# Kernel tuning notes

Measured on AMD Instinct MI355X. Metric: run time of the kernel, lower is better.

The kernel has to match this reference:

```python
import jax, jax.numpy as jnp
import numpy as np

N = 16          # num_transforms
BS = 128        # batch_size
D = 4096        # encoder dim
C, H, W = 3, 64, 64
TEMP = 0.5      # hyperparams.temperature
LAM_H = 1.0     # hyperparams.h
EPS = 1e-8      # torch CosineSimilarity eps


def setup_inputs() -> dict:
    key = jax.random.key(0)
    k1, k2, k3 = jax.random.split(key, 3)
    return {
        "pic_set": jax.random.normal(k1, (N, BS, C, H, W), dtype=jnp.float32),
        "dec_pics": jax.random.normal(k2, (N, BS, C, H, W), dtype=jnp.float32),
        "h": jax.random.normal(k3, (N, BS, D), dtype=jnp.float32),
    }


def _pos_neg_indices(n, bs):
    # Static (numpy) index construction replicating the boolean masks.
    # Positives of row i: all j != i with j % bs == i % bs (sorted, row-major),
    # Negatives of row i: all j with j % bs != i % bs (sorted).
    k = n * bs
    i = np.arange(k)
    cols = (i % bs)[:, None] + np.arange(n)[None, :] * bs          # (K, N)
    pos_idx = cols[cols != i[:, None]].reshape(k, n - 1)            # (K, N-1)
    jj = np.arange(k)
    neg_mask = (jj[None, :] % bs) != (i[:, None] % bs)              # (K, K)
    neg_idx = np.broadcast_to(jj, (k, k))[neg_mask].reshape(k, k - n)  # (K, K-N)
    return jnp.asarray(pos_idx), jnp.asarray(neg_idx)


def _nt_xent(h):
    n, bs, d = h.shape
    k = n * bs
    s = h.reshape(k, d)
    # CosineSimilarity(dim=2) with eps clamp on norms
    nrm = jnp.maximum(jnp.linalg.norm(s, axis=1), EPS)
    sn = s / nrm[:, None]
    simmat = (sn @ sn.T) / TEMP                                     # (K, K)
    pos_idx, neg_idx = _pos_neg_indices(n, bs)
    pos = jnp.take_along_axis(simmat, pos_idx, axis=1)              # (K, N-1)
    neg = jnp.take_along_axis(simmat, neg_idx, axis=1)              # (K, K-N)
    # CrossEntropyLoss(reduction='sum') with label 0 on logits
    # [pos_{i,m}, neg_i] == sum of logsumexp - pos; logsumexp over concat
    # factors as logaddexp(lse(neg_i), pos_{i,m}).
    neg_lse = jax.scipy.special.logsumexp(neg, axis=1)              # (K,)
    loss = jnp.sum(jnp.logaddexp(neg_lse[:, None], pos) - pos)
    kpos = k * (n - 1)
    return loss / kpos


def reference(pic_set, dec_pics, h):
    n, bs = pic_set.shape[0], pic_set.shape[1]
    loss_h = _nt_xent(h)
    # dec_pics[(i+1) % N] cyclic offset, then flat MSE (mean reduction)
    offset = (np.arange(n) + 1) % n
    p = pic_set.reshape(n, bs, -1)
    dshift = dec_pics.reshape(n, bs, -1)[offset]
    loss_pairs = jnp.mean((p - dshift) ** 2)
    return loss_pairs + LAM_H * loss_h
```

## Files before the change

### kernel.cpp

```cpp
#include <hip/hip_runtime.h>
#include <hip/hip_bf16.h>
#include <math.h>

#define N_T   16
#define BSZ   128
#define DDIM  4096
#define KROWS (N_T * BSZ)
#define CHW   (3 * 64 * 64)
#define S_PIC (BSZ * CHW)
#define T_MSE (N_T * S_PIC)
#define KPOS  (KROWS * (N_T - 1))

#define MSE_BLOCKS  3072

typedef short  bf16x8 __attribute__((ext_vector_type(8)));
typedef float  f32x4  __attribute__((ext_vector_type(4)));

__device__ __forceinline__ float waveReduceSum(float v) {
    for (int off = 32; off > 0; off >>= 1) v += __shfl_down(v, off, 64);
    return v;
}
__device__ __forceinline__ float blockReduceSum(float v) {
    __shared__ float s[8];
    int lane = threadIdx.x & 63, wid = threadIdx.x >> 6;
    v = waveReduceSum(v);
    if (lane == 0) s[wid] = v;
    __syncthreads();
    int nw = (blockDim.x + 63) >> 6;
    v = (threadIdx.x < nw) ? s[threadIdx.x] : 0.0f;
    if (wid == 0) v = waveReduceSum(v);
    return v;
}

__device__ __forceinline__ void mse_block(const float* __restrict__ pic,
                                          const float* __restrict__ dec,
                                          float* __restrict__ acc,
                                          int n, int bx) {
    const size_t off = (size_t)n * S_PIC + (size_t)bx * 8192 + threadIdx.x * 4;
    const ptrdiff_t doff = (ptrdiff_t)(((n + 1) & (N_T - 1)) - n) * S_PIC;
    const float* p = pic + off;
    const float* d = dec + off + doff;
    float s0 = 0.f, s1 = 0.f, s2 = 0.f, s3 = 0.f;
#pragma unroll
    for (int k = 0; k < 8; k++) {
        float4 a = *(const float4*)(p + k * 1024);
        float4 b = *(const float4*)(d + k * 1024);
        float dx = a.x - b.x, dy = a.y - b.y, dz = a.z - b.z, dw = a.w - b.w;
        s0 += dx * dx; s1 += dy * dy; s2 += dz * dz; s3 += dw * dw;
    }
    float sum = (s0 + s1) + (s2 + s3);
    sum = blockReduceSum(sum);
    if (threadIdx.x == 0) atomicAdd(acc, sum);
}

__global__ void norm_kernel(const float* __restrict__ h,
                            __hip_bfloat16* __restrict__ hb,
                            float* __restrict__ acc, int zero_acc) {
    if (zero_acc && blockIdx.x == 0 && threadIdx.x < 64)
        acc[threadIdx.x] = 0.0f;

    const int row = blockIdx.x;
    const float* r = h + (size_t)row * DDIM;
    float ss = 0.0f;
    for (int k = threadIdx.x * 8; k < DDIM; k += blockDim.x * 8) {
        float4 v0 = *(const float4*)(r + k);
        float4 v1 = *(const float4*)(r + k + 4);
        ss += v0.x * v0.x + v0.y * v0.y + v0.z * v0.z + v0.w * v0.w;
        ss += v1.x * v1.x + v1.y * v1.y + v1.z * v1.z + v1.w * v1.w;
    }
    ss = blockReduceSum(ss);
    __shared__ float scale_s;
    if (threadIdx.x == 0) scale_s = 1.0f / fmaxf(sqrtf(ss), 1e-8f);
    __syncthreads();
    const float sc = scale_s;
    __hip_bfloat16* ob = hb + (size_t)row * DDIM;
    for (int k = threadIdx.x * 8; k < DDIM; k += blockDim.x * 8) {
        float4 v0 = *(const float4*)(r + k);
        float4 v1 = *(const float4*)(r + k + 4);
        __hip_bfloat16 t[8];
        t[0] = __float2bfloat16(v0.x * sc); t[1] = __float2bfloat16(v0.y * sc);
        t[2] = __float2bfloat16(v0.z * sc); t[3] = __float2bfloat16(v0.w * sc);
        t[4] = __float2bfloat16(v1.x * sc); t[5] = __float2bfloat16(v1.y * sc);
        t[6] = __float2bfloat16(v1.z * sc); t[7] = __float2bfloat16(v1.w * sc);
        *(bf16x8*)(ob + k) = *(const bf16x8*)t;
    }
}

template<int NKZ>
__global__ __launch_bounds__(256) void mega_kernel(const ushort* __restrict__ X,
                                                   float* __restrict__ Cpart,
                                                   const float* __restrict__ pic,
                                                   const float* __restrict__ dec,
                                                   float* __restrict__ acc) {
    __shared__ ushort As[128 * 32];
    __shared__ ushort Bs[128 * 32];
    constexpr int NG = NKZ * 256;
    int bid = blockIdx.x;

    if (bid >= NG) {
        const int t = bid - NG;
        mse_block(pic, dec, acc, t & (N_T - 1), t >> 4);
        return;
    }

    bid = (bid & 7) * (NG >> 3) + (bid >> 3);

    const int kz = bid >> 8;
    const int bi = (bid >> 4) & 15, bj = bid & 15;
    const int tid  = threadIdx.x;
    const int wave = tid >> 6, lane = tid & 63;
    const int wm = wave >> 1, wn = wave & 1;
    const int quad = lane >> 4, l16 = lane & 15;

    f32x4 acc_r[4][4];
#pragma unroll
    for (int i = 0; i < 4; i++)
#pragma unroll
        for (int j = 0; j < 4; j++) acc_r[i][j] = (f32x4){0.f, 0.f, 0.f, 0.f};

    const int srow = lane >> 2;
    const int scol = (lane & 3) * 8;
    const ushort* Ag0 = X + (size_t)(bi * 128 + wave * 16       + srow) * DDIM + scol;
    const ushort* Ag1 = X + (size_t)(bi * 128 + (wave + 4) * 16 + srow) * DDIM + scol;
    const ushort* Bg0 = X + (size_t)(bj * 128 + wave * 16       + srow) * DDIM + scol;
    const ushort* Bg1 = X + (size_t)(bj * 128 + (wave + 4) * 16 + srow) * DDIM + scol;
    ushort* Al0 = As + wave * 512;
    ushort* Al1 = As + (wave + 4) * 512;
    ushort* Bl0 = Bs + wave * 512;
    ushort* Bl1 = Bs + (wave + 4) * 512;

    constexpr int KS = DDIM / NKZ;
    const int k0 = kz * KS, k1 = k0 + KS;
    for (int kk = k0; kk < k1; kk += 32) {
        __syncthreads();
        __builtin_amdgcn_global_load_lds(
            (const __attribute__((address_space(1))) unsigned int*)(Ag0 + kk),
            (__attribute__((address_space(3))) unsigned int*)Al0, 16, 0, 0);
        __builtin_amdgcn_global_load_lds(
            (const __attribute__((address_space(1))) unsigned int*)(Ag1 + kk),
            (__attribute__((address_space(3))) unsigned int*)Al1, 16, 0, 0);
        __builtin_amdgcn_global_load_lds(
            (const __attribute__((address_space(1))) unsigned int*)(Bg0 + kk),
            (__attribute__((address_space(3))) unsigned int*)Bl0, 16, 0, 0);
        __builtin_amdgcn_global_load_lds(
            (const __attribute__((address_space(1))) unsigned int*)(Bg1 + kk),
            (__attribute__((address_space(3))) unsigned int*)Bl1, 16, 0, 0);
        __syncthreads();

        bf16x8 a[4], b[4];
#pragma unroll
        for (int t = 0; t < 4; t++)
            a[t] = *(const bf16x8*)(As + (wm * 64 + t * 16 + l16) * 32 + quad * 8);
#pragma unroll
        for (int t = 0; t < 4; t++)
            b[t] = *(const bf16x8*)(Bs + (wn * 64 + t * 16 + l16) * 32 + quad * 8);
#pragma unroll
        for (int mt = 0; mt < 4; mt++)
#pragma unroll
            for (int nt = 0; nt < 4; nt++)
                acc_r[mt][nt] = __builtin_amdgcn_mfma_f32_16x16x32_bf16(
                    a[mt], b[nt], acc_r[mt][nt], 0, 0, 0);
    }

    float* Cp = Cpart + (size_t)kz * KROWS * KROWS;
#pragma unroll
    for (int mt = 0; mt < 4; mt++) {
#pragma unroll
        for (int r = 0; r < 4; r++) {
            const int row = bi * 128 + wm * 64 + mt * 16 + quad * 4 + r;
            float* o = Cp + (size_t)row * KROWS + bj * 128 + wn * 64 + l16;
#pragma unroll
            for (int nt = 0; nt < 4; nt++) o[nt * 16] = 2.0f * acc_r[mt][nt][r];
        }
    }
}

__global__ __launch_bounds__(256) void mse_kernel(const float* __restrict__ pic,
                                                  const float* __restrict__ dec,
                                                  float* __restrict__ acc) {
    mse_block(pic, dec, acc, blockIdx.y, blockIdx.x);
}

template<int NKZ>
__global__ void lse_kernel(const float* __restrict__ Cpart,
                           float* __restrict__ acc,
                           float* __restrict__ out) {
    const int i = blockIdx.x;
    __shared__ float srow[KROWS];
    const float* r0 = Cpart + (size_t)i * KROWS;
    for (int j = threadIdx.x * 4; j < KROWS; j += blockDim.x * 4) {
        float4 s = *(const float4*)(r0 + j);
#pragma unroll
        for (int p = 1; p < NKZ; p++) {
            float4 b = *(const float4*)(r0 + (size_t)p * KROWS * KROWS + j);
            s.x += b.x; s.y += b.y; s.z += b.z; s.w += b.w;
        }
        *(float4*)(srow + j) = s;
    }
    __syncthreads();

    const int ires = i & (BSZ - 1);
    float se = 0.0f;
    for (int j = threadIdx.x; j < KROWS; j += blockDim.x)
        if ((j & (BSZ - 1)) != ires) se += __expf(srow[j] - 2.0f);
    se = blockReduceSum(se);

    if (threadIdx.x == 0) {
        const float neg_lse = 2.0f + __logf(se);
        float loss = 0.0f;
#pragma unroll
        for (int t = 0; t < N_T; t++) {
            const int j = ires + t * BSZ;
            if (j == i) continue;
            const float x = neg_lse - srow[j];
            loss += (x > 0.0f) ? (x + log1pf(expf(-x))) : log1pf(expf(x));
        }
        atomicAdd(acc + 1, loss);
        __threadfence();
        const int old = atomicAdd((int*)acc + 8, 1);
        if (old == KROWS - 1) {
            const float mse = atomicAdd(acc + 0, 0.0f);
            const float lh  = atomicAdd(acc + 1, 0.0f);
            out[0] = mse / (float)T_MSE + lh / (float)KPOS;
        }
    }
}

extern "C" void kernel_launch(void* const* d_in, const int* in_sizes, int n_in,
                              void* d_out, int out_size, void* d_ws, size_t ws_size,
                              hipStream_t stream) {
    const float* pic = (const float*)d_in[0];
    float* dec = (float*)d_in[1];
    const float* h = (const float*)d_in[2];
    float* out = (float*)d_out;

    float* acc = (float*)d_ws;
    const size_t hbuf_bytes = (size_t)KROWS * DDIM * sizeof(__hip_bfloat16);
    const size_t part_bytes = (size_t)KROWS * KROWS * sizeof(float);

    if (ws_size >= 256 + hbuf_bytes + 4 * part_bytes) {
        __hip_bfloat16* hbuf = (__hip_bfloat16*)((char*)d_ws + 256);
        float* Cpart = (float*)((char*)d_ws + 256 + hbuf_bytes);
        norm_kernel<<<KROWS, 256, 0, stream>>>(h, hbuf, acc, 1);
        mega_kernel<4><<<4 * 256 + MSE_BLOCKS, 256, 0, stream>>>(
            (const ushort*)hbuf, Cpart, pic, dec, acc);
        lse_kernel<4><<<KROWS, 256, 0, stream>>>(Cpart, acc, out);
    } else if (ws_size >= 256 + hbuf_bytes + 2 * part_bytes) {
        __hip_bfloat16* hbuf = (__hip_bfloat16*)((char*)d_ws + 256);
        float* Cpart = (float*)((char*)d_ws + 256 + hbuf_bytes);
        norm_kernel<<<KROWS, 256, 0, stream>>>(h, hbuf, acc, 1);
        mega_kernel<2><<<2 * 256 + MSE_BLOCKS, 256, 0, stream>>>(
            (const ushort*)hbuf, Cpart, pic, dec, acc);
        lse_kernel<2><<<KROWS, 256, 0, stream>>>(Cpart, acc, out);
    } else {
        hipMemsetAsync(d_ws, 0, 256, stream);
        __hip_bfloat16* hbuf = (__hip_bfloat16*)dec;
        float* Cpart = (float*)((char*)dec + hbuf_bytes);
        mse_kernel<<<dim3(MSE_BLOCKS / N_T, N_T), 256, 0, stream>>>(pic, dec, acc);
        norm_kernel<<<KROWS, 256, 0, stream>>>(h, hbuf, acc, 0);
        mega_kernel<2><<<2 * 256, 256, 0, stream>>>(
            (const ushort*)hbuf, Cpart, pic, dec, acc);
        lse_kernel<2><<<KROWS, 256, 0, stream>>>(Cpart, acc, out);
    }
}
```

Before: 345.2 us.

## Fuse norm, GEMM, MSE and LSE into one persistent kernel with grid barriers

```diff
diff --git a/kernel.cpp b/kernel.cpp
--- a/kernel.cpp
+++ b/kernel.cpp
@@ -11,6 +11,8 @@
 #define T_MSE (N_T * S_PIC)
 #define KPOS  (KROWS * (N_T - 1))
 
+#define NBLK        1024
+#define MSE_JOBS    3072
 #define MSE_BLOCKS  3072
 
 typedef short  bf16x8 __attribute__((ext_vector_type(8)));
@@ -22,25 +24,44 @@
 }
 __device__ __forceinline__ float blockReduceSum(float v) {
     __shared__ float s[8];
+    __syncthreads();
     int lane = threadIdx.x & 63, wid = threadIdx.x >> 6;
     v = waveReduceSum(v);
     if (lane == 0) s[wid] = v;
     __syncthreads();
-    int nw = (blockDim.x + 63) >> 6;
-    v = (threadIdx.x < nw) ? s[threadIdx.x] : 0.0f;
+    v = (threadIdx.x < 4) ? s[threadIdx.x] : 0.0f;
     if (wid == 0) v = waveReduceSum(v);
     return v;
 }
 
-__device__ __forceinline__ void mse_block(const float* __restrict__ pic,
-                                          const float* __restrict__ dec,
-                                          float* __restrict__ acc,
-                                          int n, int bx) {
+__device__ __forceinline__ void grid_sync(int* cnt, int* gen) {
+    __syncthreads();
+    __threadfence();
+    __syncthreads();
+    if (threadIdx.x == 0) {
+        const int g = __hip_atomic_load(gen, __ATOMIC_RELAXED, __HIP_MEMORY_SCOPE_AGENT);
+        if (__hip_atomic_fetch_add(cnt, 1, __ATOMIC_ACQ_REL, __HIP_MEMORY_SCOPE_AGENT)
+            == NBLK - 1) {
+            __hip_atomic_store(cnt, 0, __ATOMIC_RELAXED, __HIP_MEMORY_SCOPE_AGENT);
+            __hip_atomic_fetch_add(gen, 1, __ATOMIC_RELEASE, __HIP_MEMORY_SCOPE_AGENT);
+        } else {
+            while (__hip_atomic_load(gen, __ATOMIC_ACQUIRE, __HIP_MEMORY_SCOPE_AGENT) == g)
+                __builtin_amdgcn_s_sleep(8);
+        }
+    }
+    __syncthreads();
+    __threadfence();
+}
+
+__device__ __forceinline__ void mse_job(const float* __restrict__ pic,
+                                        const float* __restrict__ dec,
+                                        int t, float& s0, float& s1,
+                                        float& s2, float& s3) {
+    const int n = t & (N_T - 1), bx = t >> 4;
     const size_t off = (size_t)n * S_PIC + (size_t)bx * 8192 + threadIdx.x * 4;
     const ptrdiff_t doff = (ptrdiff_t)(((n + 1) & (N_T - 1)) - n) * S_PIC;
     const float* p = pic + off;
     const float* d = dec + off + doff;
-    float s0 = 0.f, s1 = 0.f, s2 = 0.f, s3 = 0.f;
 #pragma unroll
     for (int k = 0; k < 8; k++) {
         float4 a = *(const float4*)(p + k * 1024);
@@ -48,8 +69,189 @@
         float dx = a.x - b.x, dy = a.y - b.y, dz = a.z - b.z, dw = a.w - b.w;
         s0 += dx * dx; s1 += dy * dy; s2 += dz * dz; s3 += dw * dw;
     }
-    float sum = (s0 + s1) + (s2 + s3);
-    sum = blockReduceSum(sum);
+}
+
+__global__ __launch_bounds__(256, 4) void fused_kernel(
+        const float* __restrict__ pic, const float* __restrict__ dec,
+        const float* __restrict__ h, __hip_bfloat16* __restrict__ hbuf,
+        float* __restrict__ Cpart, float* __restrict__ acc,
+        int* __restrict__ bar, float* __restrict__ out) {
+    __shared__ ushort As[128 * 32];
+    __shared__ ushort Bs[128 * 32];
+    __shared__ float scale_s;
+    const int tid = threadIdx.x;
+    int* const cnt = bar;
+    int* const gen = bar + 1;
+
+    {
+        const ushort* hu = (const ushort*)h;
+        (void)hu;
+#pragma unroll
+        for (int rr = 0; rr < 2; rr++) {
+            const int row = (blockIdx.x << 1) | rr;
+            const float* rp = h + (size_t)row * DDIM + tid * 16;
+            float4 v0 = *(const float4*)(rp);
+            float4 v1 = *(const float4*)(rp + 4);
+            float4 v2 = *(const float4*)(rp + 8);
+            float4 v3 = *(const float4*)(rp + 12);
+            float ss = v0.x * v0.x + v0.y * v0.y + v0.z * v0.z + v0.w * v0.w
+                     + v1.x * v1.x + v1.y * v1.y + v1.z * v1.z + v1.w * v1.w
+                     + v2.x * v2.x + v2.y * v2.y + v2.z * v2.z + v2.w * v2.w
+                     + v3.x * v3.x + v3.y * v3.y + v3.z * v3.z + v3.w * v3.w;
+            ss = blockReduceSum(ss);
+            if (tid == 0) scale_s = 1.0f / fmaxf(sqrtf(ss), 1e-8f);
+            __syncthreads();
+            const float sc = scale_s;
+            __hip_bfloat16 t[16];
+            t[0]  = __float2bfloat16(v0.x * sc); t[1]  = __float2bfloat16(v0.y * sc);
+            t[2]  = __float2bfloat16(v0.z * sc); t[3]  = __float2bfloat16(v0.w * sc);
+            t[4]  = __float2bfloat16(v1.x * sc); t[5]  = __float2bfloat16(v1.y * sc);
+            t[6]  = __float2bfloat16(v1.z * sc); t[7]  = __float2bfloat16(v1.w * sc);
+            t[8]  = __float2bfloat16(v2.x * sc); t[9]  = __float2bfloat16(v2.y * sc);
+            t[10] = __float2bfloat16(v2.z * sc); t[11] = __float2bfloat16(v2.w * sc);
+            t[12] = __float2bfloat16(v3.x * sc); t[13] = __float2bfloat16(v3.y * sc);
+            t[14] = __float2bfloat16(v3.z * sc); t[15] = __float2bfloat16(v3.w * sc);
+            __hip_bfloat16* ob = hbuf + (size_t)row * DDIM + tid * 16;
+            *(bf16x8*)(ob)     = *(const bf16x8*)(t);
+            *(bf16x8*)(ob + 8) = *(const bf16x8*)(t + 8);
+        }
+        float s0 = 0.f, s1 = 0.f, s2 = 0.f, s3 = 0.f;
+#pragma unroll
+        for (int q = 0; q < 3; q++)
+            mse_job(pic, dec, blockIdx.x * 3 + q, s0, s1, s2, s3);
+        float msum = blockReduceSum((s0 + s1) + (s2 + s3));
+        if (tid == 0) atomicAdd(acc, msum);
+    }
+
+    grid_sync(cnt, gen);
+
+    {
+        int bid = blockIdx.x;
+        bid = (bid & 7) * (NBLK >> 3) + (bid >> 3);
+        const int kz = bid >> 8;
+        const int bi = (bid >> 4) & 15, bj = bid & 15;
+        const int wave = tid >> 6, lane = tid & 63;
+        const int wm = wave >> 1, wn = wave & 1;
+        const int quad = lane >> 4, l16 = lane & 15;
+        const ushort* X = (const ushort*)hbuf;
+
+        f32x4 acc_r[4][4];
+#pragma unroll
+        for (int i = 0; i < 4; i++)
+#pragma unroll
+            for (int j = 0; j < 4; j++) acc_r[i][j] = (f32x4){0.f, 0.f, 0.f, 0.f};
+
+        const int srw = lane >> 2;
+        const int scl = (lane & 3) * 8;
+        const ushort* Ag0 = X + (size_t)(bi * 128 + wave * 16       + srw) * DDIM + scl;
+        const ushort* Ag1 = X + (size_t)(bi * 128 + (wave + 4) * 16 + srw) * DDIM + scl;
+        const ushort* Bg0 = X + (size_t)(bj * 128 + wave * 16       + srw) * DDIM + scl;
+        const ushort* Bg1 = X + (size_t)(bj * 128 + (wave + 4) * 16 + srw) * DDIM + scl;
+        ushort* Al0 = As + wave * 512;
+        ushort* Al1 = As + (wave + 4) * 512;
+        ushort* Bl0 = Bs + wave * 512;
+        ushort* Bl1 = Bs + (wave + 4) * 512;
+
+        const int k0 = kz * (DDIM / 4), k1 = k0 + (DDIM / 4);
+        for (int kk = k0; kk < k1; kk += 32) {
+            __syncthreads();
+            __builtin_amdgcn_global_load_lds(
+                (const __attribute__((address_space(1))) unsigned int*)(Ag0 + kk),
+                (__attribute__((address_space(3))) unsigned int*)Al0, 16, 0, 0);
+            __builtin_amdgcn_global_load_lds(
+                (const __attribute__((address_space(1))) unsigned int*)(Ag1 + kk),
+                (__attribute__((address_space(3))) unsigned int*)Al1, 16, 0, 0);
+            __builtin_amdgcn_global_load_lds(
+                (const __attribute__((address_space(1))) unsigned int*)(Bg0 + kk),
+                (__attribute__((address_space(3))) unsigned int*)Bl0, 16, 0, 0);
+            __builtin_amdgcn_global_load_lds(
+                (const __attribute__((address_space(1))) unsigned int*)(Bg1 + kk),
+                (__attribute__((address_space(3))) unsigned int*)Bl1, 16, 0, 0);
+            __syncthreads();
+
+            bf16x8 a[4], b[4];
+#pragma unroll
+            for (int t = 0; t < 4; t++)
+                a[t] = *(const bf16x8*)(As + (wm * 64 + t * 16 + l16) * 32 + quad * 8);
+#pragma unroll
+            for (int t = 0; t < 4; t++)
+                b[t] = *(const bf16x8*)(Bs + (wn * 64 + t * 16 + l16) * 32 + quad * 8);
+#pragma unroll
+            for (int mt = 0; mt < 4; mt++)
+#pragma unroll
+                for (int nt = 0; nt < 4; nt++)
+                    acc_r[mt][nt] = __builtin_amdgcn_mfma_f32_16x16x32_bf16(
+                        a[mt], b[nt], acc_r[mt][nt], 0, 0, 0);
+        }
+
+        float* Cp = Cpart + (size_t)kz * KROWS * KROWS;
+#pragma unroll
+        for (int mt = 0; mt < 4; mt++) {
+#pragma unroll
+            for (int r = 0; r < 4; r++) {
+                const int row = bi * 128 + wm * 64 + mt * 16 + quad * 4 + r;
+                float* o = Cp + (size_t)row * KROWS + bj * 128 + wn * 64 + l16;
+#pragma unroll
+                for (int nt = 0; nt < 4; nt++) o[nt * 16] = 2.0f * acc_r[mt][nt][r];
+            }
+        }
+    }
+
+    grid_sync(cnt, gen);
+
+    {
+        float* srow = (float*)As;
+        float lsum = 0.0f;
+#pragma unroll
+        for (int rr = 0; rr < 2; rr++) {
+            const int i = (blockIdx.x << 1) | rr;
+            __syncthreads();
+            const float* r0 = Cpart + (size_t)i * KROWS;
+            for (int j = tid * 4; j < KROWS; j += 1024) {
+                float4 s = *(const float4*)(r0 + j);
+#pragma unroll
+                for (int p = 1; p < 4; p++) {
+                    const float4 b = *(const float4*)(r0 + (size_t)p * KROWS * KROWS + j);
+                    s.x += b.x; s.y += b.y; s.z += b.z; s.w += b.w;
+                }
+                *(float4*)(srow + j) = s;
+            }
+            __syncthreads();
+            const int ires = i & (BSZ - 1);
+            float se = 0.0f;
+            for (int j = tid; j < KROWS; j += 256)
+                if ((j & (BSZ - 1)) != ires) se += __expf(srow[j] - 2.0f);
+            se = blockReduceSum(se);
+            if (tid == 0) {
+                const float neg_lse = 2.0f + __logf(se);
+#pragma unroll
+                for (int t = 0; t < N_T; t++) {
+                    const int j = ires + t * BSZ;
+                    if (j == i) continue;
+                    const float x = neg_lse - srow[j];
+                    lsum += (x > 0.0f) ? (x + log1pf(expf(-x))) : log1pf(expf(x));
+                }
+            }
+        }
+        if (tid == 0) atomicAdd(acc + 1, lsum);
+    }
+
+    grid_sync(cnt, gen);
+
+    if (blockIdx.x == 0 && threadIdx.x == 0) {
+        const float mse = atomicAdd(acc + 0, 0.0f);
+        const float lh  = atomicAdd(acc + 1, 0.0f);
+        out[0] = mse / (float)T_MSE + lh / (float)KPOS;
+    }
+}
+
+__device__ __forceinline__ void mse_block(const float* __restrict__ pic,
+                                          const float* __restrict__ dec,
+                                          float* __restrict__ acc,
+                                          int n, int bx) {
+    float s0 = 0.f, s1 = 0.f, s2 = 0.f, s3 = 0.f;
+    mse_job(pic, dec, (bx << 4) | n, s0, s1, s2, s3);
+    float sum = blockReduceSum((s0 + s1) + (s2 + s3));
     if (threadIdx.x == 0) atomicAdd(acc, sum);
 }
 
@@ -58,7 +260,6 @@
                             float* __restrict__ acc, int zero_acc) {
     if (zero_acc && blockIdx.x == 0 && threadIdx.x < 64)
         acc[threadIdx.x] = 0.0f;
-
     const int row = blockIdx.x;
     const float* r = h + (size_t)row * DDIM;
     float ss = 0.0f;
@@ -96,39 +297,33 @@
     __shared__ ushort Bs[128 * 32];
     constexpr int NG = NKZ * 256;
     int bid = blockIdx.x;
-
     if (bid >= NG) {
         const int t = bid - NG;
         mse_block(pic, dec, acc, t & (N_T - 1), t >> 4);
         return;
     }
-
     bid = (bid & 7) * (NG >> 3) + (bid >> 3);
-
     const int kz = bid >> 8;
     const int bi = (bid >> 4) & 15, bj = bid & 15;
-    const int tid  = threadIdx.x;
+    const int tid = threadIdx.x;
     const int wave = tid >> 6, lane = tid & 63;
     const int wm = wave >> 1, wn = wave & 1;
     const int quad = lane >> 4, l16 = lane & 15;
-
     f32x4 acc_r[4][4];
 #pragma unroll
     for (int i = 0; i < 4; i++)
 #pragma unroll
         for (int j = 0; j < 4; j++) acc_r[i][j] = (f32x4){0.f, 0.f, 0.f, 0.f};
-
-    const int srow = lane >> 2;
-    const int scol = (lane & 3) * 8;
-    const ushort* Ag0 = X + (size_t)(bi * 128 + wave * 16       + srow) * DDIM + scol;
-    const ushort* Ag1 = X + (size_t)(bi * 128 + (wave + 4) * 16 + srow) * DDIM + scol;
-    const ushort* Bg0 = X + (size_t)(bj * 128 + wave * 16       + srow) * DDIM + scol;
-    const ushort* Bg1 = X + (size_t)(bj * 128 + (wave + 4) * 16 + srow) * DDIM + scol;
+    const int srw = lane >> 2;
+    const int scl = (lane & 3) * 8;
+    const ushort* Ag0 = X + (size_t)(bi * 128 + wave * 16       + srw) * DDIM + scl;
+    const ushort* Ag1 = X + (size_t)(bi * 128 + (wave + 4) * 16 + srw) * DDIM + scl;
+    const ushort* Bg0 = X + (size_t)(bj * 128 + wave * 16       + srw) * DDIM + scl;
+    const ushort* Bg1 = X + (size_t)(bj * 128 + (wave + 4) * 16 + srw) * DDIM + scl;
     ushort* Al0 = As + wave * 512;
     ushort* Al1 = As + (wave + 4) * 512;
     ushort* Bl0 = Bs + wave * 512;
     ushort* Bl1 = Bs + (wave + 4) * 512;
-
     constexpr int KS = DDIM / NKZ;
     const int k0 = kz * KS, k1 = k0 + KS;
     for (int kk = k0; kk < k1; kk += 32) {
@@ -146,7 +341,6 @@
             (const __attribute__((address_space(1))) unsigned int*)(Bg1 + kk),
             (__attribute__((address_space(3))) unsigned int*)Bl1, 16, 0, 0);
         __syncthreads();
-
         bf16x8 a[4], b[4];
 #pragma unroll
         for (int t = 0; t < 4; t++)
@@ -161,7 +355,6 @@
                 acc_r[mt][nt] = __builtin_amdgcn_mfma_f32_16x16x32_bf16(
                     a[mt], b[nt], acc_r[mt][nt], 0, 0, 0);
     }
-
     float* Cp = Cpart + (size_t)kz * KROWS * KROWS;
 #pragma unroll
     for (int mt = 0; mt < 4; mt++) {
@@ -198,13 +391,11 @@
         *(float4*)(srow + j) = s;
     }
     __syncthreads();
-
     const int ires = i & (BSZ - 1);
     float se = 0.0f;
     for (int j = threadIdx.x; j < KROWS; j += blockDim.x)
         if ((j & (BSZ - 1)) != ires) se += __expf(srow[j] - 2.0f);
     se = blockReduceSum(se);
-
     if (threadIdx.x == 0) {
         const float neg_lse = 2.0f + __logf(se);
         float loss = 0.0f;
@@ -235,16 +426,15 @@
     float* out = (float*)d_out;
 
     float* acc = (float*)d_ws;
+    int* bar = (int*)d_ws + 32;
     const size_t hbuf_bytes = (size_t)KROWS * DDIM * sizeof(__hip_bfloat16);
     const size_t part_bytes = (size_t)KROWS * KROWS * sizeof(float);
 
     if (ws_size >= 256 + hbuf_bytes + 4 * part_bytes) {
         __hip_bfloat16* hbuf = (__hip_bfloat16*)((char*)d_ws + 256);
         float* Cpart = (float*)((char*)d_ws + 256 + hbuf_bytes);
-        norm_kernel<<<KROWS, 256, 0, stream>>>(h, hbuf, acc, 1);
-        mega_kernel<4><<<4 * 256 + MSE_BLOCKS, 256, 0, stream>>>(
-            (const ushort*)hbuf, Cpart, pic, dec, acc);
-        lse_kernel<4><<<KROWS, 256, 0, stream>>>(Cpart, acc, out);
+        hipMemsetAsync(d_ws, 0, 256, stream);
+        fused_kernel<<<NBLK, 256, 0, stream>>>(pic, dec, h, hbuf, Cpart, acc, bar, out);
     } else if (ws_size >= 256 + hbuf_bytes + 2 * part_bytes) {
         __hip_bfloat16* hbuf = (__hip_bfloat16*)((char*)d_ws + 256);
         float* Cpart = (float*)((char*)d_ws + 256 + hbuf_bytes);
```

Result: slower. 1.359 ms (+293.6%).

## Double-buffer GEMM LDS tiles, drop 4-way split-K path, flatten norm kernel

Applied to the files above, without the earlier changes.

```diff
diff --git a/kernel.cpp b/kernel.cpp
--- a/kernel.cpp
+++ b/kernel.cpp
@@ -53,37 +53,40 @@
     if (threadIdx.x == 0) atomicAdd(acc, sum);
 }
 
-__global__ void norm_kernel(const float* __restrict__ h,
-                            __hip_bfloat16* __restrict__ hb,
-                            float* __restrict__ acc, int zero_acc) {
+__global__ __launch_bounds__(256) void norm_kernel(const float* __restrict__ h,
+                                                   __hip_bfloat16* __restrict__ hb,
+                                                   float* __restrict__ acc,
+                                                   int zero_acc) {
     if (zero_acc && blockIdx.x == 0 && threadIdx.x < 64)
         acc[threadIdx.x] = 0.0f;
 
     const int row = blockIdx.x;
-    const float* r = h + (size_t)row * DDIM;
-    float ss = 0.0f;
-    for (int k = threadIdx.x * 8; k < DDIM; k += blockDim.x * 8) {
-        float4 v0 = *(const float4*)(r + k);
-        float4 v1 = *(const float4*)(r + k + 4);
-        ss += v0.x * v0.x + v0.y * v0.y + v0.z * v0.z + v0.w * v0.w;
-        ss += v1.x * v1.x + v1.y * v1.y + v1.z * v1.z + v1.w * v1.w;
-    }
+    const float* rp = h + (size_t)row * DDIM + threadIdx.x * 16;
+    float4 v0 = *(const float4*)(rp);
+    float4 v1 = *(const float4*)(rp + 4);
+    float4 v2 = *(const float4*)(rp + 8);
+    float4 v3 = *(const float4*)(rp + 12);
+    float ss = v0.x * v0.x + v0.y * v0.y + v0.z * v0.z + v0.w * v0.w
+             + v1.x * v1.x + v1.y * v1.y + v1.z * v1.z + v1.w * v1.w
+             + v2.x * v2.x + v2.y * v2.y + v2.z * v2.z + v2.w * v2.w
+             + v3.x * v3.x + v3.y * v3.y + v3.z * v3.z + v3.w * v3.w;
     ss = blockReduceSum(ss);
     __shared__ float scale_s;
     if (threadIdx.x == 0) scale_s = 1.0f / fmaxf(sqrtf(ss), 1e-8f);
     __syncthreads();
     const float sc = scale_s;
-    __hip_bfloat16* ob = hb + (size_t)row * DDIM;
-    for (int k = threadIdx.x * 8; k < DDIM; k += blockDim.x * 8) {
-        float4 v0 = *(const float4*)(r + k);
-        float4 v1 = *(const float4*)(r + k + 4);
-        __hip_bfloat16 t[8];
-        t[0] = __float2bfloat16(v0.x * sc); t[1] = __float2bfloat16(v0.y * sc);
-        t[2] = __float2bfloat16(v0.z * sc); t[3] = __float2bfloat16(v0.w * sc);
-        t[4] = __float2bfloat16(v1.x * sc); t[5] = __float2bfloat16(v1.y * sc);
-        t[6] = __float2bfloat16(v1.z * sc); t[7] = __float2bfloat16(v1.w * sc);
-        *(bf16x8*)(ob + k) = *(const bf16x8*)t;
-    }
+    __hip_bfloat16 t[16];
+    t[0]  = __float2bfloat16(v0.x * sc); t[1]  = __float2bfloat16(v0.y * sc);
+    t[2]  = __float2bfloat16(v0.z * sc); t[3]  = __float2bfloat16(v0.w * sc);
+    t[4]  = __float2bfloat16(v1.x * sc); t[5]  = __float2bfloat16(v1.y * sc);
+    t[6]  = __float2bfloat16(v1.z * sc); t[7]  = __float2bfloat16(v1.w * sc);
+    t[8]  = __float2bfloat16(v2.x * sc); t[9]  = __float2bfloat16(v2.y * sc);
+    t[10] = __float2bfloat16(v2.z * sc); t[11] = __float2bfloat16(v2.w * sc);
+    t[12] = __float2bfloat16(v3.x * sc); t[13] = __float2bfloat16(v3.y * sc);
+    t[14] = __float2bfloat16(v3.z * sc); t[15] = __float2bfloat16(v3.w * sc);
+    __hip_bfloat16* ob = hb + (size_t)row * DDIM + threadIdx.x * 16;
+    *(bf16x8*)(ob)     = *(const bf16x8*)(t);
+    *(bf16x8*)(ob + 8) = *(const bf16x8*)(t + 8);
 }
 
 template<int NKZ>
@@ -92,8 +95,10 @@
                                                    const float* __restrict__ pic,
                                                    const float* __restrict__ dec,
                                                    float* __restrict__ acc) {
-    __shared__ ushort As[128 * 32];
-    __shared__ ushort Bs[128 * 32];
+    __shared__ ushort As0[128 * 32];
+    __shared__ ushort Bs0[128 * 32];
+    __shared__ ushort As1[128 * 32];
+    __shared__ ushort Bs1[128 * 32];
     constexpr int NG = NKZ * 256;
     int bid = blockIdx.x;
 
@@ -118,48 +123,63 @@
 #pragma unroll
         for (int j = 0; j < 4; j++) acc_r[i][j] = (f32x4){0.f, 0.f, 0.f, 0.f};
 
-    const int srow = lane >> 2;
-    const int scol = (lane & 3) * 8;
-    const ushort* Ag0 = X + (size_t)(bi * 128 + wave * 16       + srow) * DDIM + scol;
-    const ushort* Ag1 = X + (size_t)(bi * 128 + (wave + 4) * 16 + srow) * DDIM + scol;
-    const ushort* Bg0 = X + (size_t)(bj * 128 + wave * 16       + srow) * DDIM + scol;
-    const ushort* Bg1 = X + (size_t)(bj * 128 + (wave + 4) * 16 + srow) * DDIM + scol;
-    ushort* Al0 = As + wave * 512;
-    ushort* Al1 = As + (wave + 4) * 512;
-    ushort* Bl0 = Bs + wave * 512;
-    ushort* Bl1 = Bs + (wave + 4) * 512;
-
-    constexpr int KS = DDIM / NKZ;
-    const int k0 = kz * KS, k1 = k0 + KS;
-    for (int kk = k0; kk < k1; kk += 32) {
-        __syncthreads();
+    const int srw = lane >> 2;
+    const int scl = (lane & 3) * 8;
+    const ushort* Ag0 = X + (size_t)(bi * 128 + wave * 16       + srw) * DDIM + scl;
+    const ushort* Ag1 = X + (size_t)(bi * 128 + (wave + 4) * 16 + srw) * DDIM + scl;
+    const ushort* Bg0 = X + (size_t)(bj * 128 + wave * 16       + srw) * DDIM + scl;
+    const ushort* Bg1 = X + (size_t)(bj * 128 + (wave + 4) * 16 + srw) * DDIM + scl;
+
+    auto stage = [&](ushort* Al, ushort* Bl, int kk) {
         __builtin_amdgcn_global_load_lds(
             (const __attribute__((address_space(1))) unsigned int*)(Ag0 + kk),
-            (__attribute__((address_space(3))) unsigned int*)Al0, 16, 0, 0);
+            (__attribute__((address_space(3))) unsigned int*)(Al + wave * 512), 16, 0, 0);
         __builtin_amdgcn_global_load_lds(
             (const __attribute__((address_space(1))) unsigned int*)(Ag1 + kk),
-            (__attribute__((address_space(3))) unsigned int*)Al1, 16, 0, 0);
+            (__attribute__((address_space(3))) unsigned int*)(Al + (wave + 4) * 512), 16, 0, 0);
         __builtin_amdgcn_global_load_lds(
             (const __attribute__((address_space(1))) unsigned int*)(Bg0 + kk),
-            (__attribute__((address_space(3))) unsigned int*)Bl0, 16, 0, 0);
+            (__attribute__((address_space(3))) unsigned int*)(Bl + wave * 512), 16, 0, 0);
         __builtin_amdgcn_global_load_lds(
             (const __attribute__((address_space(1))) unsigned int*)(Bg1 + kk),
-            (__attribute__((address_space(3))) unsigned int*)Bl1, 16, 0, 0);
-        __syncthreads();
-
+            (__attribute__((address_space(3))) unsigned int*)(Bl + (wave + 4) * 512), 16, 0, 0);
+    };
+    auto compute = [&](const ushort* Al, const ushort* Bl) {
         bf16x8 a[4], b[4];
 #pragma unroll
         for (int t = 0; t < 4; t++)
-            a[t] = *(const bf16x8*)(As + (wm * 64 + t * 16 + l16) * 32 + quad * 8);
+            a[t] = *(const bf16x8*)(Al + (wm * 64 + t * 16 + l16) * 32 + quad * 8);
 #pragma unroll
         for (int t = 0; t < 4; t++)
-            b[t] = *(const bf16x8*)(Bs + (wn * 64 + t * 16 + l16) * 32 + quad * 8);
+            b[t] = *(const bf16x8*)(Bl + (wn * 64 + t * 16 + l16) * 32 + quad * 8);
 #pragma unroll
         for (int mt = 0; mt < 4; mt++)
 #pragma unroll
             for (int nt = 0; nt < 4; nt++)
                 acc_r[mt][nt] = __builtin_amdgcn_mfma_f32_16x16x32_bf16(
                     a[mt], b[nt], acc_r[mt][nt], 0, 0, 0);
+    };
+
+    constexpr int KS = DDIM / NKZ;
+    const int k0 = kz * KS, k1 = k0 + KS;
+
+    stage(As0, Bs0, k0);
+    asm volatile("s_waitcnt vmcnt(0)" ::: "memory");
+    __builtin_amdgcn_s_barrier();
+
+    for (int kk = k0; kk < k1; kk += 64) {
+        stage(As1, Bs1, kk + 32);
+        compute(As0, Bs0);
+        asm volatile("s_waitcnt vmcnt(0)" ::: "memory");
+        __builtin_amdgcn_s_barrier();
+        if (kk + 64 < k1) {
+            stage(As0, Bs0, kk + 64);
+            compute(As1, Bs1);
+            asm volatile("s_waitcnt vmcnt(0)" ::: "memory");
+            __builtin_amdgcn_s_barrier();
+        } else {
+            compute(As1, Bs1);
+        }
     }
 
     float* Cp = Cpart + (size_t)kz * KROWS * KROWS;
@@ -238,14 +258,7 @@
     const size_t hbuf_bytes = (size_t)KROWS * DDIM * sizeof(__hip_bfloat16);
     const size_t part_bytes = (size_t)KROWS * KROWS * sizeof(float);
 
-    if (ws_size >= 256 + hbuf_bytes + 4 * part_bytes) {
-        __hip_bfloat16* hbuf = (__hip_bfloat16*)((char*)d_ws + 256);
-        float* Cpart = (float*)((char*)d_ws + 256 + hbuf_bytes);
-        norm_kernel<<<KROWS, 256, 0, stream>>>(h, hbuf, acc, 1);
-        mega_kernel<4><<<4 * 256 + MSE_BLOCKS, 256, 0, stream>>>(
-            (const ushort*)hbuf, Cpart, pic, dec, acc);
-        lse_kernel<4><<<KROWS, 256, 0, stream>>>(Cpart, acc, out);
-    } else if (ws_size >= 256 + hbuf_bytes + 2 * part_bytes) {
+    if (ws_size >= 256 + hbuf_bytes + 2 * part_bytes) {
         __hip_bfloat16* hbuf = (__hip_bfloat16*)((char*)d_ws + 256);
         float* Cpart = (float*)((char*)d_ws + 256 + hbuf_bytes);
         norm_kernel<<<KROWS, 256, 0, stream>>>(h, hbuf, acc, 1);
```

After: 338.9 us. No clear change (-1.8%).
